# Kernel tuning notes

Hardware: AMD Instinct MI355X
Metric: run time of the kernel (lower is better)

The kernel has to match this reference:

```python
import jax, jax.numpy as jnp
import numpy as np

D_MODEL = 1024

def setup_inputs() -> dict:
    key = jax.random.key(0)
    ks = jax.random.split(key, 5)
    s = 1.0 / np.sqrt(D_MODEL)  # torch Linear default init scale-ish
    x = jax.random.normal(ks[0], (4, 2048, D_MODEL), dtype=jnp.float32)
    Wq = jax.random.normal(ks[1], (D_MODEL, D_MODEL), dtype=jnp.float32) * s
    Wk = jax.random.normal(ks[2], (D_MODEL, D_MODEL), dtype=jnp.float32) * s
    Wv = jax.random.normal(ks[3], (D_MODEL, D_MODEL), dtype=jnp.float32) * s
    Wo = jax.random.normal(ks[4], (D_MODEL, D_MODEL), dtype=jnp.float32) * s
    z = jnp.zeros((D_MODEL,), dtype=jnp.float32)
    return {"x": x, "Wq": Wq, "bq": z, "Wk": Wk, "bk": z, "Wv": Wv, "bv": z, "Wo": Wo, "bo": z}

def reference(x, Wq, bq, Wk, bk, Wv, bv, Wo, bo):
    # x: (B, S, D). Single-head causal attention, dropout in eval mode (identity).
    B, S, D = x.shape
    Q = jnp.einsum('bsd,ed->bse', x, Wq) + bq
    K = jnp.einsum('bsd,ed->bse', x, Wk) + bk
    V = jnp.einsum('bsd,ed->bse', x, Wv) + bv
    scores = jnp.einsum('bqd,bkd->bqk', Q, K) / jnp.sqrt(jnp.float32(D))
    causal = jnp.tril(jnp.ones((S, S), dtype=bool))  # (S, S)
    scores = jnp.where(causal, scores, -jnp.inf)
    weights = jax.nn.softmax(scores, axis=-1)
    attended = jnp.einsum('bqk,bkd->bqd', weights, V)
    out = jnp.einsum('bsd,ed->bse', attended, Wo) + bo
    return out
```

## Files before the change

### kernel.cpp

```cpp
#include <hip/hip_runtime.h>
#include <cstdint>
#include <cstddef>


#define D_MODEL 1024
#define SEQ     2048
#define BATCH   4

typedef unsigned short u16;
typedef __bf16 bf16_t;
typedef bf16_t bf16x8 __attribute__((ext_vector_type(8)));
typedef float  f32x4  __attribute__((ext_vector_type(4)));
typedef u16    u16x4  __attribute__((ext_vector_type(4)));

__device__ __forceinline__ u16 f2bf(float x) {
  union { float f; uint32_t u; } v; v.f = x;
  uint32_t r = v.u + 0x7fffu + ((v.u >> 16) & 1u);
  return (u16)(r >> 16);
}

__device__ __forceinline__ void gload_lds16(const u16* g, u16* l) {
  __builtin_amdgcn_global_load_lds((__attribute__((address_space(1))) void*)g,
                                   (__attribute__((address_space(3))) void*)l,
                                   16, 0, 0);
}

template <bool ROWSUM>
__device__ __forceinline__ void gemm_core(const u16* __restrict__ Ablk,
                                          const u16* __restrict__ Bblk,
                                          int lda, int ldb, int ksteps32,
                                          u16* As, u16* Bs,
                                          f32x4 acc[4][4], f32x4* rs) {
  const int tid  = threadIdx.x;
  const int wave = tid >> 6, lane = tid & 63;
  const int wr = (wave >> 1) * 64, wc = (wave & 1) * 64;
  const int frow = lane & 15, kc = lane >> 4;
  const int ch0 = tid, ch1 = 256 + tid;
  const int m0 = ch0 >> 2, k80 = (((ch0 & 3) ^ ((m0 >> 1) & 3))) * 8;
  const int m1 = ch1 >> 2, k81 = (((ch1 & 3) ^ ((m1 >> 1) & 3))) * 8;
  int aoff[4], boff[4];
#pragma unroll
  for (int i = 0; i < 4; ++i) {
    const int ra = wr + i * 16 + frow;
    aoff[i] = (ra * 4 + (kc ^ ((ra >> 1) & 3))) * 8;
    const int rb = wc + i * 16 + frow;
    boff[i] = (rb * 4 + (kc ^ ((rb >> 1) & 3))) * 8;
  }
  bf16x8 ones;
  if (ROWSUM) {
#pragma unroll
    for (int r = 0; r < 8; ++r) ((u16*)&ones)[r] = 0x3F80;
  }

  for (int kt = 0; kt < ksteps32; ++kt) {
    __syncthreads();
    const int kb = kt * 32;
    gload_lds16(Ablk + m0 * lda + kb + k80, As + ch0 * 8);
    gload_lds16(Ablk + m1 * lda + kb + k81, As + ch1 * 8);
    gload_lds16(Bblk + m0 * ldb + kb + k80, Bs + ch0 * 8);
    gload_lds16(Bblk + m1 * ldb + kb + k81, Bs + ch1 * 8);
    asm volatile("s_waitcnt vmcnt(0)" ::: "memory");
    __syncthreads();

    bf16x8 af[4], bf[4];
#pragma unroll
    for (int i = 0; i < 4; ++i) af[i] = *(const bf16x8*)(As + aoff[i]);
#pragma unroll
    for (int j = 0; j < 4; ++j) bf[j] = *(const bf16x8*)(Bs + boff[j]);
#pragma unroll
    for (int i = 0; i < 4; ++i)
#pragma unroll
      for (int j = 0; j < 4; ++j)
        acc[i][j] = __builtin_amdgcn_mfma_f32_16x16x32_bf16(af[i], bf[j], acc[i][j], 0, 0, 0);
    if (ROWSUM) {
#pragma unroll
      for (int i = 0; i < 4; ++i)
        rs[i] = __builtin_amdgcn_mfma_f32_16x16x32_bf16(af[i], ones, rs[i], 0, 0, 0);
    }
  }
}

__global__ __launch_bounds__(256) void cvt_kernel(const float4* __restrict__ x,
                                                  const float4* __restrict__ wq,
                                                  const float4* __restrict__ wk,
                                                  const float4* __restrict__ wv,
                                                  const float4* __restrict__ wo,
                                                  u16* __restrict__ dst) {
  const int i = blockIdx.x * 256 + threadIdx.x;
  float4 v;
  if (i < 2097152) {
    v = x[i];
  } else {
    const int j = i - 2097152;
    const int w = j >> 18;
    const float4* s = (w == 0) ? wq : (w == 1) ? wk : (w == 2) ? wv : wo;
    v = s[j & 262143];
  }
  u16x4 o = {f2bf(v.x), f2bf(v.y), f2bf(v.z), f2bf(v.w)};
  *(u16x4*)(dst + (size_t)i * 4) = o;
}

__global__ void transposeW_kernel(const u16* __restrict__ src, u16* __restrict__ dst) {
  __shared__ u16 tile[32][33];
  const int r0 = blockIdx.x * 32, c0 = blockIdx.y * 32;
  const int tx = threadIdx.x, ty = threadIdx.y;
#pragma unroll
  for (int r = 0; r < 4; ++r)
    tile[ty + r * 8][tx] = src[(size_t)(r0 + ty + r * 8) * D_MODEL + c0 + tx];
  __syncthreads();
#pragma unroll
  for (int r = 0; r < 4; ++r)
    dst[(size_t)(c0 + ty + r * 8) * D_MODEL + r0 + tx] = tile[tx][ty + r * 8];
}

__global__ __launch_bounds__(256) void stageA_kernel(
    const u16* __restrict__ xb,
    const u16* __restrict__ WqB, const u16* __restrict__ WkB,
    const u16* __restrict__ WoB, const u16* __restrict__ WvT,
    const float* __restrict__ Wo32, const float* __restrict__ bv,
    const float* __restrict__ bq, const float* __restrict__ bk,
    u16* __restrict__ Qb, u16* __restrict__ Kb,
    u16* __restrict__ Wp, float* __restrict__ bp) {
  __shared__ __align__(16) u16 As[4096];
  __shared__ __align__(16) u16 Bs[4096];
  const int blk = blockIdx.x;
  const int lane = threadIdx.x & 63, wave = threadIdx.x >> 6;
  const int wr = (wave >> 1) * 64, wc = (wave & 1) * 64;
  const int cl = lane & 15, rl = (lane >> 4) * 4;

  if (blk < 64) {
    const int f0 = (blk >> 3) * 128, e0 = (blk & 7) * 128;
    f32x4 acc[4][4] = {};
    gemm_core<false>(WoB + (size_t)f0 * D_MODEL, WvT + (size_t)e0 * D_MODEL,
                     D_MODEL, D_MODEL, 32, As, Bs, acc, nullptr);
#pragma unroll
    for (int j = 0; j < 4; ++j) {
      const int col = e0 + wc + j * 16 + cl;
#pragma unroll
      for (int i = 0; i < 4; ++i)
#pragma unroll
        for (int r = 0; r < 4; ++r) {
          const int row = f0 + wr + i * 16 + rl + r;
          Wp[(size_t)row * D_MODEL + col] = f2bf(acc[i][j][r]);
        }
    }
  } else if (blk < 80) {
    const int f = (blk - 64) * 64 + (threadIdx.x >> 2);
    const int dq = threadIdx.x & 3;
    const float* row = Wo32 + (size_t)f * D_MODEL + dq * 256;
    const float* bvq = bv + dq * 256;
    float s = 0.f;
#pragma unroll 8
    for (int i = 0; i < 256; ++i) s += row[i] * bvq[i];
    s += __shfl_xor(s, 1);
    s += __shfl_xor(s, 2);
    if (dq == 0) bp[f] = s;
  } else {
    const int v = blk - 80;
    const int c = v & 7, s = v >> 3;
    const int row0 = (c * 8 + (s >> 4)) * 128;
    const int cz = s & 15;
    const int z = cz >> 3;
    const int col0 = (cz & 7) * 128;
    const u16*   W    = z ? WkB : WqB;
    const float* bias = z ? bk : bq;
    u16*         out  = z ? Kb : Qb;
    f32x4 acc[4][4] = {};
    gemm_core<false>(xb + (size_t)row0 * D_MODEL, W + (size_t)col0 * D_MODEL,
                     D_MODEL, D_MODEL, 32, As, Bs, acc, nullptr);
#pragma unroll
    for (int j = 0; j < 4; ++j) {
      const int col = col0 + wc + j * 16 + cl;
      const float bb = bias[col];
#pragma unroll
      for (int i = 0; i < 4; ++i)
#pragma unroll
        for (int r = 0; r < 4; ++r) {
          const int row = row0 + wr + i * 16 + rl + r;
          out[(size_t)row * D_MODEL + col] = f2bf(acc[i][j][r] + bb);
        }
    }
  }
}

__global__ __launch_bounds__(256) void stageB_kernel(
    const u16* __restrict__ xb, const u16* __restrict__ Wp,
    const float* __restrict__ bp,
    const u16* __restrict__ Qb, const u16* __restrict__ Kb,
    u16* __restrict__ Vt, u16* __restrict__ Eb) {
  __shared__ __align__(16) u16 As[4096];
  __shared__ __align__(16) u16 Bs[4096];
  const int blk = blockIdx.x;
  const int lane = threadIdx.x & 63, wave = threadIdx.x >> 6;
  const int wr = (wave >> 1) * 64, wc = (wave & 1) * 64;
  const int cl = lane & 15, rl = (lane >> 4) * 4;

  if (blk < 544) {
    const int c = blk & 7, s = blk >> 3;
    int b, qi, ji;
    if (s < 48) {
      static const int sq_tab[6] = {1, 2, 2, 3, 3, 3};
      static const int sj_tab[6] = {0, 0, 1, 0, 1, 2};
      const int fi = c * 3 + (s >> 4);
      const int off = s & 15;
      b = fi / 6;
      const int fs = fi % 6;
      qi = sq_tab[fs] * 4 + (off >> 2);
      ji = sj_tab[fs] * 4 + (off & 3);
    } else {
      static const int di_tab[10] = {0, 1, 1, 2, 2, 2, 3, 3, 3, 3};
      static const int dj_tab[10] = {0, 0, 1, 0, 1, 2, 0, 1, 2, 3};
      const int k = (s - 48) / 10;
      const int off = (s - 48) % 10;
      const int di = c * 2 + k;
      b = di >> 2;
      const int dk = di & 3;
      qi = dk * 4 + di_tab[off];
      ji = dk * 4 + dj_tab[off];
    }
    const u16* A  = Qb + (size_t)(b * SEQ + qi * 128) * D_MODEL;
    const u16* Bt = Kb + (size_t)(b * SEQ + ji * 128) * D_MODEL;
    f32x4 acc[4][4] = {};
    gemm_core<false>(A, Bt, D_MODEL, D_MODEL, 32, As, Bs, acc, nullptr);
    u16* out = Eb + (size_t)b * SEQ * SEQ;
#pragma unroll
    for (int i = 0; i < 4; ++i)
#pragma unroll
      for (int r = 0; r < 4; ++r) {
        const int q = qi * 128 + wr + i * 16 + rl + r;
#pragma unroll
        for (int j = 0; j < 4; ++j) {
          const int jj = ji * 128 + wc + j * 16 + cl;
          out[(size_t)q * SEQ + jj] =
              (jj <= q) ? f2bf(__expf(acc[i][j][r] * 0.03125f)) : (u16)0;
        }
      }
  } else {
    const int v = blk - 544;
    const int c = v & 7, s = v >> 3;
    const int row0 = (c * 8 + (s >> 3)) * 128;
    const int col0 = (s & 7) * 128;
    f32x4 acc[4][4] = {};
    gemm_core<false>(xb + (size_t)row0 * D_MODEL, Wp + (size_t)col0 * D_MODEL,
                     D_MODEL, D_MODEL, 32, As, Bs, acc, nullptr);
    const int b = row0 >> 11;
    u16* vt = Vt + (size_t)b * D_MODEL * SEQ;
#pragma unroll
    for (int j = 0; j < 4; ++j) {
      const int col = col0 + wc + j * 16 + cl;
      const float bb = bp[col];
#pragma unroll
      for (int i = 0; i < 4; ++i) {
        const int s0 = (row0 & 2047) + wr + i * 16 + rl;
        u16x4 o = {f2bf(acc[i][j][0] + bb), f2bf(acc[i][j][1] + bb),
                   f2bf(acc[i][j][2] + bb), f2bf(acc[i][j][3] + bb)};
        *(u16x4*)(vt + (size_t)col * SEQ + s0) = o;
      }
    }
  }
}

__global__ __launch_bounds__(256) void pv_kernel(const u16* __restrict__ Eb,
                                                 const u16* __restrict__ Vt,
                                                 const float* __restrict__ bo,
                                                 float* __restrict__ Out) {
  __shared__ __align__(16) u16 As[4096];
  __shared__ __align__(16) u16 Bs[4096];
  const int u = blockIdx.x;
  const int c = u & 7, s = u >> 3;
  const int b  = c >> 1;
  const int dt = (c & 1) * 4 + (s >> 4);
  const int qt = 15 - (s & 15);
  const u16* A  = Eb + (size_t)b * SEQ * SEQ + (size_t)(qt * 128) * SEQ;
  const u16* Bt = Vt + (size_t)b * D_MODEL * SEQ + (size_t)(dt * 128) * SEQ;
  f32x4 acc[4][4] = {};
  f32x4 rs[4] = {};
  gemm_core<true>(A, Bt, SEQ, SEQ, (qt + 1) * 4, As, Bs, acc, rs);
  const int lane = threadIdx.x & 63, wave = threadIdx.x >> 6;
  const int wr = (wave >> 1) * 64, wc = (wave & 1) * 64;
  const int cl = lane & 15, rl = (lane >> 4) * 4;
#pragma unroll
  for (int i = 0; i < 4; ++i)
#pragma unroll
    for (int r = 0; r < 4; ++r) {
      const float invl = 1.0f / rs[i][r];
      const int row = b * SEQ + qt * 128 + wr + i * 16 + rl + r;
#pragma unroll
      for (int j = 0; j < 4; ++j) {
        const int col = dt * 128 + wc + j * 16 + cl;
        Out[(size_t)row * D_MODEL + col] = acc[i][j][r] * invl + bo[col];
      }
    }
}

extern "C" void kernel_launch(void* const* d_in, const int* in_sizes, int n_in,
                              void* d_out, int out_size, void* d_ws, size_t ws_size,
                              hipStream_t stream) {
  const float* x  = (const float*)d_in[0];
  const float* Wq = (const float*)d_in[1];
  const float* bq = (const float*)d_in[2];
  const float* Wk = (const float*)d_in[3];
  const float* bk = (const float*)d_in[4];
  const float* Wv = (const float*)d_in[5];
  const float* bv = (const float*)d_in[6];
  const float* Wo = (const float*)d_in[7];
  const float* bo = (const float*)d_in[8];
  float* out = (float*)d_out;
  char* ws = (char*)d_ws;

  u16*   xb  = (u16*)(ws);
  u16*   Wb  = (u16*)(ws + (16u << 20));
  u16*   Qb  = (u16*)(ws + (24u << 20));
  u16*   Kb  = (u16*)(ws + (40u << 20));
  u16*   Vt  = (u16*)(ws + (56u << 20));
  u16*   Eb  = (u16*)(ws + (72u << 20));
  u16*   WvT = (u16*)(ws + (104u << 20));
  u16*   Wp  = (u16*)(ws + (106u << 20));
  float* bp  = (float*)(ws + (108u << 20));

  cvt_kernel<<<12288, 256, 0, stream>>>((const float4*)x, (const float4*)Wq,
                                        (const float4*)Wk, (const float4*)Wv,
                                        (const float4*)Wo, xb);
  transposeW_kernel<<<dim3(32, 32), dim3(32, 8), 0, stream>>>(Wb + (2u << 20), WvT);
  stageA_kernel<<<1104, 256, 0, stream>>>(xb, Wb, Wb + (1u << 20), Wb + (3u << 20),
                                          WvT, Wo, bv, bq, bk, Qb, Kb, Wp, bp);
  stageB_kernel<<<1056, 256, 0, stream>>>(xb, Wp, bp, Qb, Kb, Vt, Eb);
  pv_kernel<<<512, 256, 0, stream>>>(Eb, Vt, bo, out);
}
```

Before: 267.9 us.

## Pipeline GEMM core with 4-stage LDS ring and enlarge tiles to 128x256

The shared GEMM core now prefetches K-slices two steps ahead into a four-deep LDS ring using vmcnt-based waits, and raises wave priority around the MFMA block. Block tiles grow from 128x128 with 4 waves to 128x256 with 8 waves, and all three stages are remapped to the new tiling: stage A fuses the QK projection with the Wv·Wo and bias work, stage B merges triangular score tiles, and PV is rebalanced. The aim is to hide global-load latency, which the old single-buffered loop exposed, and to raise operand reuse per block. In exchange it uses much more LDS per block, which may limit occupancy, and the block-to-work mapping becomes more complex.

```diff
diff --git a/kernel.cpp b/kernel.cpp
--- a/kernel.cpp
+++ b/kernel.cpp
@@ -26,24 +26,26 @@
 }
 
 template <bool ROWSUM>
-__device__ __forceinline__ void gemm_core(const u16* __restrict__ Ablk,
-                                          const u16* __restrict__ Bblk,
-                                          int lda, int ldb, int ksteps32,
+__device__ __forceinline__ void gemm_core(const u16* __restrict__ A,
+                                          const u16* __restrict__ B,
+                                          int lda, int ldb, int nt,
                                           u16* As, u16* Bs,
                                           f32x4 acc[4][4], f32x4* rs) {
   const int tid  = threadIdx.x;
-  const int wave = tid >> 6, lane = tid & 63;
-  const int wr = (wave >> 1) * 64, wc = (wave & 1) * 64;
+  const int lane = tid & 63, wave = tid >> 6;
   const int frow = lane & 15, kc = lane >> 4;
-  const int ch0 = tid, ch1 = 256 + tid;
-  const int m0 = ch0 >> 2, k80 = (((ch0 & 3) ^ ((m0 >> 1) & 3))) * 8;
-  const int m1 = ch1 >> 2, k81 = (((ch1 & 3) ^ ((m1 >> 1) & 3))) * 8;
+  const int abase = (wave >> 2) * 64, bbase = (wave & 3) * 64;
+  const int ar = tid >> 2;
+  const int ac = (tid & 3) ^ ((ar >> 1) & 3);
+  const u16* Asrc  = A + (size_t)ar * lda + ac * 8;
+  const u16* Bsrc0 = B + (size_t)ar * ldb + ac * 8;
+  const u16* Bsrc1 = B + (size_t)(ar + 128) * ldb + ac * 8;
   int aoff[4], boff[4];
 #pragma unroll
   for (int i = 0; i < 4; ++i) {
-    const int ra = wr + i * 16 + frow;
+    const int ra = abase + i * 16 + frow;
     aoff[i] = (ra * 4 + (kc ^ ((ra >> 1) & 3))) * 8;
-    const int rb = wc + i * 16 + frow;
+    const int rb = bbase + i * 16 + frow;
     boff[i] = (rb * 4 + (kc ^ ((rb >> 1) & 3))) * 8;
   }
   bf16x8 ones;
@@ -51,22 +53,30 @@
 #pragma unroll
     for (int r = 0; r < 8; ++r) ((u16*)&ones)[r] = 0x3F80;
   }
-
-  for (int kt = 0; kt < ksteps32; ++kt) {
-    __syncthreads();
-    const int kb = kt * 32;
-    gload_lds16(Ablk + m0 * lda + kb + k80, As + ch0 * 8);
-    gload_lds16(Ablk + m1 * lda + kb + k81, As + ch1 * 8);
-    gload_lds16(Bblk + m0 * ldb + kb + k80, Bs + ch0 * 8);
-    gload_lds16(Bblk + m1 * ldb + kb + k81, Bs + ch1 * 8);
-    asm volatile("s_waitcnt vmcnt(0)" ::: "memory");
-    __syncthreads();
-
+  auto stage = [&](int t) {
+    u16* ab = As + (t & 3) * 4096;
+    u16* bb = Bs + (t & 3) * 8192;
+    const int kb = t * 32;
+    gload_lds16(Asrc + kb, ab + tid * 8);
+    gload_lds16(Bsrc0 + kb, bb + tid * 8);
+    gload_lds16(Bsrc1 + kb, bb + 4096 + tid * 8);
+  };
+  stage(0);
+  stage(1);
+  for (int t = 0; t < nt; ++t) {
+    if (t + 1 < nt) asm volatile("s_waitcnt vmcnt(3)" ::: "memory");
+    else            asm volatile("s_waitcnt vmcnt(0)" ::: "memory");
+    if (t + 2 < nt) stage(t + 2);
+    __builtin_amdgcn_s_barrier();
+    asm volatile("" ::: "memory");
+    const u16* ab = As + (t & 3) * 4096;
+    const u16* bb = Bs + (t & 3) * 8192;
     bf16x8 af[4], bf[4];
 #pragma unroll
-    for (int i = 0; i < 4; ++i) af[i] = *(const bf16x8*)(As + aoff[i]);
-#pragma unroll
-    for (int j = 0; j < 4; ++j) bf[j] = *(const bf16x8*)(Bs + boff[j]);
+    for (int i = 0; i < 4; ++i) af[i] = *(const bf16x8*)(ab + aoff[i]);
+#pragma unroll
+    for (int j = 0; j < 4; ++j) bf[j] = *(const bf16x8*)(bb + boff[j]);
+    __builtin_amdgcn_s_setprio(1);
 #pragma unroll
     for (int i = 0; i < 4; ++i)
 #pragma unroll
@@ -77,6 +87,8 @@
       for (int i = 0; i < 4; ++i)
         rs[i] = __builtin_amdgcn_mfma_f32_16x16x32_bf16(af[i], ones, rs[i], 0, 0, 0);
     }
+    __builtin_amdgcn_s_setprio(0);
+    __builtin_amdgcn_s_barrier();
   }
 }
 
@@ -113,7 +125,7 @@
     dst[(size_t)(c0 + ty + r * 8) * D_MODEL + r0 + tx] = tile[tx][ty + r * 8];
 }
 
-__global__ __launch_bounds__(256) void stageA_kernel(
+__global__ __launch_bounds__(512, 2) void stageA_kernel(
     const u16* __restrict__ xb,
     const u16* __restrict__ WqB, const u16* __restrict__ WkB,
     const u16* __restrict__ WoB, const u16* __restrict__ WvT,
@@ -121,47 +133,18 @@
     const float* __restrict__ bq, const float* __restrict__ bk,
     u16* __restrict__ Qb, u16* __restrict__ Kb,
     u16* __restrict__ Wp, float* __restrict__ bp) {
-  __shared__ __align__(16) u16 As[4096];
-  __shared__ __align__(16) u16 Bs[4096];
-  const int blk = blockIdx.x;
-  const int lane = threadIdx.x & 63, wave = threadIdx.x >> 6;
-  const int wr = (wave >> 1) * 64, wc = (wave & 1) * 64;
+  __shared__ __align__(16) u16 As[16384];
+  __shared__ __align__(16) u16 Bs[32768];
+  const int blk = blockIdx.x, tid = threadIdx.x;
+  const int lane = tid & 63, wave = tid >> 6;
+  const int abase = (wave >> 2) * 64, bbase = (wave & 3) * 64;
   const int cl = lane & 15, rl = (lane >> 4) * 4;
-
-  if (blk < 64) {
-    const int f0 = (blk >> 3) * 128, e0 = (blk & 7) * 128;
-    f32x4 acc[4][4] = {};
-    gemm_core<false>(WoB + (size_t)f0 * D_MODEL, WvT + (size_t)e0 * D_MODEL,
-                     D_MODEL, D_MODEL, 32, As, Bs, acc, nullptr);
-#pragma unroll
-    for (int j = 0; j < 4; ++j) {
-      const int col = e0 + wc + j * 16 + cl;
-#pragma unroll
-      for (int i = 0; i < 4; ++i)
-#pragma unroll
-        for (int r = 0; r < 4; ++r) {
-          const int row = f0 + wr + i * 16 + rl + r;
-          Wp[(size_t)row * D_MODEL + col] = f2bf(acc[i][j][r]);
-        }
-    }
-  } else if (blk < 80) {
-    const int f = (blk - 64) * 64 + (threadIdx.x >> 2);
-    const int dq = threadIdx.x & 3;
-    const float* row = Wo32 + (size_t)f * D_MODEL + dq * 256;
-    const float* bvq = bv + dq * 256;
-    float s = 0.f;
-#pragma unroll 8
-    for (int i = 0; i < 256; ++i) s += row[i] * bvq[i];
-    s += __shfl_xor(s, 1);
-    s += __shfl_xor(s, 2);
-    if (dq == 0) bp[f] = s;
-  } else {
-    const int v = blk - 80;
-    const int c = v & 7, s = v >> 3;
-    const int row0 = (c * 8 + (s >> 4)) * 128;
-    const int cz = s & 15;
-    const int z = cz >> 3;
-    const int col0 = (cz & 7) * 128;
+  const int c = blk & 7, i = blk >> 3;
+
+  {
+    const int rt   = c * 8 + (i & 7);
+    const int czi  = i >> 3;
+    const int row0 = rt * 128, col0 = (czi >> 1) * 256, z = czi & 1;
     const u16*   W    = z ? WkB : WqB;
     const float* bias = z ? bk : bq;
     u16*         out  = z ? Kb : Qb;
@@ -170,76 +153,95 @@
                      D_MODEL, D_MODEL, 32, As, Bs, acc, nullptr);
 #pragma unroll
     for (int j = 0; j < 4; ++j) {
-      const int col = col0 + wc + j * 16 + cl;
+      const int col = col0 + bbase + j * 16 + cl;
       const float bb = bias[col];
 #pragma unroll
-      for (int i = 0; i < 4; ++i)
+      for (int ii = 0; ii < 4; ++ii)
 #pragma unroll
         for (int r = 0; r < 4; ++r) {
-          const int row = row0 + wr + i * 16 + rl + r;
-          out[(size_t)row * D_MODEL + col] = f2bf(acc[i][j][r] + bb);
+          const int row = row0 + abase + ii * 16 + rl + r;
+          out[(size_t)row * D_MODEL + col] = f2bf(acc[ii][j][r] + bb);
         }
     }
   }
-}
-
-__global__ __launch_bounds__(256) void stageB_kernel(
+  if (i < 4) {
+    const int widx = c * 4 + i;
+    const int f0 = (widx >> 2) * 128, e0 = (widx & 3) * 256;
+    f32x4 acc[4][4] = {};
+    gemm_core<false>(WoB + (size_t)f0 * D_MODEL, WvT + (size_t)e0 * D_MODEL,
+                     D_MODEL, D_MODEL, 32, As, Bs, acc, nullptr);
+#pragma unroll
+    for (int j = 0; j < 4; ++j) {
+      const int col = e0 + bbase + j * 16 + cl;
+#pragma unroll
+      for (int ii = 0; ii < 4; ++ii)
+#pragma unroll
+        for (int r = 0; r < 4; ++r) {
+          const int row = f0 + abase + ii * 16 + rl + r;
+          Wp[(size_t)row * D_MODEL + col] = f2bf(acc[ii][j][r]);
+        }
+    }
+  } else if (i < 6) {
+    const int f  = (c * 2 + (i - 4)) * 64 + (tid >> 3);
+    const int dq = tid & 7;
+    const float* row = Wo32 + (size_t)f * D_MODEL + dq * 128;
+    const float* bvq = bv + dq * 128;
+    float s = 0.f;
+#pragma unroll 8
+    for (int k = 0; k < 128; ++k) s += row[k] * bvq[k];
+    s += __shfl_xor(s, 1);
+    s += __shfl_xor(s, 2);
+    s += __shfl_xor(s, 4);
+    if (dq == 0) bp[f] = s;
+  }
+}
+
+__global__ __launch_bounds__(512, 2) void stageB_kernel(
     const u16* __restrict__ xb, const u16* __restrict__ Wp,
     const float* __restrict__ bp,
     const u16* __restrict__ Qb, const u16* __restrict__ Kb,
     u16* __restrict__ Vt, u16* __restrict__ Eb) {
-  __shared__ __align__(16) u16 As[4096];
-  __shared__ __align__(16) u16 Bs[4096];
-  const int blk = blockIdx.x;
-  const int lane = threadIdx.x & 63, wave = threadIdx.x >> 6;
-  const int wr = (wave >> 1) * 64, wc = (wave & 1) * 64;
+  __shared__ __align__(16) u16 As[16384];
+  __shared__ __align__(16) u16 Bs[32768];
+  const int blk = blockIdx.x, tid = threadIdx.x;
+  const int lane = tid & 63, wave = tid >> 6;
+  const int abase = (wave >> 2) * 64, bbase = (wave & 3) * 64;
   const int cl = lane & 15, rl = (lane >> 4) * 4;
 
-  if (blk < 544) {
-    const int c = blk & 7, s = blk >> 3;
-    int b, qi, ji;
-    if (s < 48) {
-      static const int sq_tab[6] = {1, 2, 2, 3, 3, 3};
-      static const int sj_tab[6] = {0, 0, 1, 0, 1, 2};
-      const int fi = c * 3 + (s >> 4);
-      const int off = s & 15;
-      b = fi / 6;
-      const int fs = fi % 6;
-      qi = sq_tab[fs] * 4 + (off >> 2);
-      ji = sj_tab[fs] * 4 + (off & 3);
-    } else {
-      static const int di_tab[10] = {0, 1, 1, 2, 2, 2, 3, 3, 3, 3};
-      static const int dj_tab[10] = {0, 0, 1, 0, 1, 2, 0, 1, 2, 3};
-      const int k = (s - 48) / 10;
-      const int off = (s - 48) % 10;
-      const int di = c * 2 + k;
-      b = di >> 2;
-      const int dk = di & 3;
-      qi = dk * 4 + di_tab[off];
-      ji = dk * 4 + dj_tab[off];
-    }
-    const u16* A  = Qb + (size_t)(b * SEQ + qi * 128) * D_MODEL;
-    const u16* Bt = Kb + (size_t)(b * SEQ + ji * 128) * D_MODEL;
-    f32x4 acc[4][4] = {};
-    gemm_core<false>(A, Bt, D_MODEL, D_MODEL, 32, As, Bs, acc, nullptr);
-    u16* out = Eb + (size_t)b * SEQ * SEQ;
-#pragma unroll
-    for (int i = 0; i < 4; ++i)
-#pragma unroll
-      for (int r = 0; r < 4; ++r) {
-        const int q = qi * 128 + wr + i * 16 + rl + r;
-#pragma unroll
-        for (int j = 0; j < 4; ++j) {
-          const int jj = ji * 128 + wc + j * 16 + cl;
-          out[(size_t)q * SEQ + jj] =
-              (jj <= q) ? f2bf(__expf(acc[i][j][r] * 0.03125f)) : (u16)0;
+  if (blk < 256) {
+    const int c = blk & 7;
+    const int nunit = (blk < 224) ? 1 : 2;
+    int uid = (blk < 224) ? (blk >> 3) : (28 + ((blk - 224) >> 3) * 2);
+    for (int uu = 0; uu < nunit; ++uu, ++uid) {
+      const int w = c * 36 + uid;
+      const int b = w / 72;
+      int r = w % 72, qi = 0;
+#pragma unroll 1
+      for (; qi < 16; ++qi) { const int n = (qi >> 1) + 1; if (r < n) break; r -= n; }
+      const int ji = r;
+      const u16* A  = Qb + (size_t)(b * SEQ + qi * 128) * D_MODEL;
+      const u16* Bt = Kb + (size_t)(b * SEQ + ji * 256) * D_MODEL;
+      f32x4 acc[4][4] = {};
+      gemm_core<false>(A, Bt, D_MODEL, D_MODEL, 32, As, Bs, acc, nullptr);
+      u16* out = Eb + (size_t)b * SEQ * SEQ;
+#pragma unroll
+      for (int ii = 0; ii < 4; ++ii)
+#pragma unroll
+        for (int rr = 0; rr < 4; ++rr) {
+          const int q = qi * 128 + abase + ii * 16 + rl + rr;
+#pragma unroll
+          for (int j = 0; j < 4; ++j) {
+            const int jj = ji * 256 + bbase + j * 16 + cl;
+            out[(size_t)q * SEQ + jj] =
+                (jj <= q) ? f2bf(__expf(acc[ii][j][rr] * 0.03125f)) : (u16)0;
+          }
         }
-      }
+    }
   } else {
-    const int v = blk - 544;
+    const int v = blk - 256;
     const int c = v & 7, s = v >> 3;
-    const int row0 = (c * 8 + (s >> 3)) * 128;
-    const int col0 = (s & 7) * 128;
+    const int row0 = (c * 8 + (s >> 2)) * 128;
+    const int col0 = (s & 3) * 256;
     f32x4 acc[4][4] = {};
     gemm_core<false>(xb + (size_t)row0 * D_MODEL, Wp + (size_t)col0 * D_MODEL,
                      D_MODEL, D_MODEL, 32, As, Bs, acc, nullptr);
@@ -247,48 +249,48 @@
     u16* vt = Vt + (size_t)b * D_MODEL * SEQ;
 #pragma unroll
     for (int j = 0; j < 4; ++j) {
-      const int col = col0 + wc + j * 16 + cl;
+      const int col = col0 + bbase + j * 16 + cl;
       const float bb = bp[col];
 #pragma unroll
-      for (int i = 0; i < 4; ++i) {
-        const int s0 = (row0 & 2047) + wr + i * 16 + rl;
-        u16x4 o = {f2bf(acc[i][j][0] + bb), f2bf(acc[i][j][1] + bb),
-                   f2bf(acc[i][j][2] + bb), f2bf(acc[i][j][3] + bb)};
+      for (int ii = 0; ii < 4; ++ii) {
+        const int s0 = (row0 & 2047) + abase + ii * 16 + rl;
+        u16x4 o = {f2bf(acc[ii][j][0] + bb), f2bf(acc[ii][j][1] + bb),
+                   f2bf(acc[ii][j][2] + bb), f2bf(acc[ii][j][3] + bb)};
         *(u16x4*)(vt + (size_t)col * SEQ + s0) = o;
       }
     }
   }
 }
 
-__global__ __launch_bounds__(256) void pv_kernel(const u16* __restrict__ Eb,
-                                                 const u16* __restrict__ Vt,
-                                                 const float* __restrict__ bo,
-                                                 float* __restrict__ Out) {
-  __shared__ __align__(16) u16 As[4096];
-  __shared__ __align__(16) u16 Bs[4096];
-  const int u = blockIdx.x;
-  const int c = u & 7, s = u >> 3;
+__global__ __launch_bounds__(512, 2) void pv_kernel(const u16* __restrict__ Eb,
+                                                    const u16* __restrict__ Vt,
+                                                    const float* __restrict__ bo,
+                                                    float* __restrict__ Out) {
+  __shared__ __align__(16) u16 As[16384];
+  __shared__ __align__(16) u16 Bs[32768];
+  const int blk = blockIdx.x, tid = threadIdx.x;
+  const int c = blk & 7, i = blk >> 3;
   const int b  = c >> 1;
-  const int dt = (c & 1) * 4 + (s >> 4);
-  const int qt = 15 - (s & 15);
+  const int dt = (c & 1) * 2 + (i >> 4);
+  const int qt = i & 15;
   const u16* A  = Eb + (size_t)b * SEQ * SEQ + (size_t)(qt * 128) * SEQ;
-  const u16* Bt = Vt + (size_t)b * D_MODEL * SEQ + (size_t)(dt * 128) * SEQ;
+  const u16* Bt = Vt + (size_t)b * D_MODEL * SEQ + (size_t)(dt * 256) * SEQ;
   f32x4 acc[4][4] = {};
   f32x4 rs[4] = {};
   gemm_core<true>(A, Bt, SEQ, SEQ, (qt + 1) * 4, As, Bs, acc, rs);
-  const int lane = threadIdx.x & 63, wave = threadIdx.x >> 6;
-  const int wr = (wave >> 1) * 64, wc = (wave & 1) * 64;
+  const int lane = tid & 63, wave = tid >> 6;
+  const int abase = (wave >> 2) * 64, bbase = (wave & 3) * 64;
   const int cl = lane & 15, rl = (lane >> 4) * 4;
 #pragma unroll
-  for (int i = 0; i < 4; ++i)
+  for (int ii = 0; ii < 4; ++ii)
 #pragma unroll
     for (int r = 0; r < 4; ++r) {
-      const float invl = 1.0f / rs[i][r];
-      const int row = b * SEQ + qt * 128 + wr + i * 16 + rl + r;
+      const float invl = 1.0f / rs[ii][r];
+      const int row = b * SEQ + qt * 128 + abase + ii * 16 + rl + r;
 #pragma unroll
       for (int j = 0; j < 4; ++j) {
-        const int col = dt * 128 + wc + j * 16 + cl;
-        Out[(size_t)row * D_MODEL + col] = acc[i][j][r] * invl + bo[col];
+        const int col = dt * 256 + bbase + j * 16 + cl;
+        Out[(size_t)row * D_MODEL + col] = acc[ii][j][r] * invl + bo[col];
       }
     }
 }
@@ -322,8 +324,8 @@
                                         (const float4*)Wk, (const float4*)Wv,
                                         (const float4*)Wo, xb);
   transposeW_kernel<<<dim3(32, 32), dim3(32, 8), 0, stream>>>(Wb + (2u << 20), WvT);
-  stageA_kernel<<<1104, 256, 0, stream>>>(xb, Wb, Wb + (1u << 20), Wb + (3u << 20),
-                                          WvT, Wo, bv, bq, bk, Qb, Kb, Wp, bp);
-  stageB_kernel<<<1056, 256, 0, stream>>>(xb, Wp, bp, Qb, Kb, Vt, Eb);
-  pv_kernel<<<512, 256, 0, stream>>>(Eb, Vt, bo, out);
-}
+  stageA_kernel<<<512, 512, 0, stream>>>(xb, Wb, Wb + (1u << 20), Wb + (3u << 20),
+                                         WvT, Wo, bv, bq, bk, Qb, Kb, Wp, bp);
+  stageB_kernel<<<512, 512, 0, stream>>>(xb, Wp, bp, Qb, Kb, Vt, Eb);
+  pv_kernel<<<256, 512, 0, stream>>>(Eb, Vt, bo, out);
+}
```

Measured after the change: 324.0 us. 20.9% more time.

## Compute softmax row sums in score epilogue and rebalance PV tile order

Applied to the files above, without the earlier changes.

Softmax denominators are now accumulated in the QK^T epilogue: each exponentiated score is rounded to bf16, summed across lanes with shuffles, and added to a per-row buffer with atomics. This removes the extra ones-vector MFMAs the PV GEMM used to compute row sums. The PV grid is also reordered to pair short and long causal query tiles across the two halves of the launch, for better load balance. In exchange this adds a memset, float atomics with nondeterministic summation order, and a dependency on a workspace region at 20MB, which appears to overlap the Qb allocation starting at 24MB only if sized past 4MB (it is 32KB, so fine).

```diff
diff --git a/kernel.cpp b/kernel.cpp
--- a/kernel.cpp
+++ b/kernel.cpp
@@ -18,6 +18,10 @@
   uint32_t r = v.u + 0x7fffu + ((v.u >> 16) & 1u);
   return (u16)(r >> 16);
 }
+__device__ __forceinline__ float bf2f(u16 h) {
+  union { uint32_t u; float f; } v; v.u = (uint32_t)h << 16;
+  return v.f;
+}
 
 __device__ __forceinline__ void gload_lds16(const u16* g, u16* l) {
   __builtin_amdgcn_global_load_lds((__attribute__((address_space(1))) void*)g,
@@ -25,14 +29,14 @@
                                    16, 0, 0);
 }
 
-template <bool ROWSUM>
 __device__ __forceinline__ void gemm_core(const u16* __restrict__ Ablk,
                                           const u16* __restrict__ Bblk,
                                           int lda, int ldb, int ksteps32,
                                           u16* As, u16* Bs,
-                                          f32x4 acc[4][4], f32x4* rs) {
+                                          f32x4 acc[4][4]) {
   const int tid  = threadIdx.x;
-  const int wave = tid >> 6, lane = tid & 63;
+  const int lane = tid & 63;
+  const int wave = tid >> 6;
   const int wr = (wave >> 1) * 64, wc = (wave & 1) * 64;
   const int frow = lane & 15, kc = lane >> 4;
   const int ch0 = tid, ch1 = 256 + tid;
@@ -46,19 +50,13 @@
     const int rb = wc + i * 16 + frow;
     boff[i] = (rb * 4 + (kc ^ ((rb >> 1) & 3))) * 8;
   }
-  bf16x8 ones;
-  if (ROWSUM) {
-#pragma unroll
-    for (int r = 0; r < 8; ++r) ((u16*)&ones)[r] = 0x3F80;
-  }
-
   for (int kt = 0; kt < ksteps32; ++kt) {
     __syncthreads();
     const int kb = kt * 32;
-    gload_lds16(Ablk + m0 * lda + kb + k80, As + ch0 * 8);
-    gload_lds16(Ablk + m1 * lda + kb + k81, As + ch1 * 8);
-    gload_lds16(Bblk + m0 * ldb + kb + k80, Bs + ch0 * 8);
-    gload_lds16(Bblk + m1 * ldb + kb + k81, Bs + ch1 * 8);
+    gload_lds16(Ablk + (size_t)m0 * lda + kb + k80, As + ch0 * 8);
+    gload_lds16(Ablk + (size_t)m1 * lda + kb + k81, As + ch1 * 8);
+    gload_lds16(Bblk + (size_t)m0 * ldb + kb + k80, Bs + ch0 * 8);
+    gload_lds16(Bblk + (size_t)m1 * ldb + kb + k81, Bs + ch1 * 8);
     asm volatile("s_waitcnt vmcnt(0)" ::: "memory");
     __syncthreads();
 
@@ -72,11 +70,6 @@
 #pragma unroll
       for (int j = 0; j < 4; ++j)
         acc[i][j] = __builtin_amdgcn_mfma_f32_16x16x32_bf16(af[i], bf[j], acc[i][j], 0, 0, 0);
-    if (ROWSUM) {
-#pragma unroll
-      for (int i = 0; i < 4; ++i)
-        rs[i] = __builtin_amdgcn_mfma_f32_16x16x32_bf16(af[i], ones, rs[i], 0, 0, 0);
-    }
   }
 }
 
@@ -131,8 +124,8 @@
   if (blk < 64) {
     const int f0 = (blk >> 3) * 128, e0 = (blk & 7) * 128;
     f32x4 acc[4][4] = {};
-    gemm_core<false>(WoB + (size_t)f0 * D_MODEL, WvT + (size_t)e0 * D_MODEL,
-                     D_MODEL, D_MODEL, 32, As, Bs, acc, nullptr);
+    gemm_core(WoB + (size_t)f0 * D_MODEL, WvT + (size_t)e0 * D_MODEL,
+              D_MODEL, D_MODEL, 32, As, Bs, acc);
 #pragma unroll
     for (int j = 0; j < 4; ++j) {
       const int col = e0 + wc + j * 16 + cl;
@@ -166,8 +159,8 @@
     const float* bias = z ? bk : bq;
     u16*         out  = z ? Kb : Qb;
     f32x4 acc[4][4] = {};
-    gemm_core<false>(xb + (size_t)row0 * D_MODEL, W + (size_t)col0 * D_MODEL,
-                     D_MODEL, D_MODEL, 32, As, Bs, acc, nullptr);
+    gemm_core(xb + (size_t)row0 * D_MODEL, W + (size_t)col0 * D_MODEL,
+              D_MODEL, D_MODEL, 32, As, Bs, acc);
 #pragma unroll
     for (int j = 0; j < 4; ++j) {
       const int col = col0 + wc + j * 16 + cl;
@@ -187,7 +180,7 @@
     const u16* __restrict__ xb, const u16* __restrict__ Wp,
     const float* __restrict__ bp,
     const u16* __restrict__ Qb, const u16* __restrict__ Kb,
-    u16* __restrict__ Vt, u16* __restrict__ Eb) {
+    u16* __restrict__ Vt, u16* __restrict__ Eb, float* __restrict__ rssum) {
   __shared__ __align__(16) u16 As[4096];
   __shared__ __align__(16) u16 Bs[4096];
   const int blk = blockIdx.x;
@@ -221,19 +214,27 @@
     const u16* A  = Qb + (size_t)(b * SEQ + qi * 128) * D_MODEL;
     const u16* Bt = Kb + (size_t)(b * SEQ + ji * 128) * D_MODEL;
     f32x4 acc[4][4] = {};
-    gemm_core<false>(A, Bt, D_MODEL, D_MODEL, 32, As, Bs, acc, nullptr);
+    gemm_core(A, Bt, D_MODEL, D_MODEL, 32, As, Bs, acc);
     u16* out = Eb + (size_t)b * SEQ * SEQ;
+    float* rs = rssum + b * SEQ;
 #pragma unroll
     for (int i = 0; i < 4; ++i)
 #pragma unroll
       for (int r = 0; r < 4; ++r) {
         const int q = qi * 128 + wr + i * 16 + rl + r;
+        float ps = 0.f;
 #pragma unroll
         for (int j = 0; j < 4; ++j) {
           const int jj = ji * 128 + wc + j * 16 + cl;
-          out[(size_t)q * SEQ + jj] =
-              (jj <= q) ? f2bf(__expf(acc[i][j][r] * 0.03125f)) : (u16)0;
+          u16 h16 = (jj <= q) ? f2bf(__expf(acc[i][j][r] * 0.03125f)) : (u16)0;
+          out[(size_t)q * SEQ + jj] = h16;
+          ps += bf2f(h16);
         }
+        ps += __shfl_xor(ps, 1);
+        ps += __shfl_xor(ps, 2);
+        ps += __shfl_xor(ps, 4);
+        ps += __shfl_xor(ps, 8);
+        if (cl == 0) atomicAdd(&rs[q], ps);
       }
   } else {
     const int v = blk - 544;
@@ -241,8 +242,8 @@
     const int row0 = (c * 8 + (s >> 3)) * 128;
     const int col0 = (s & 7) * 128;
     f32x4 acc[4][4] = {};
-    gemm_core<false>(xb + (size_t)row0 * D_MODEL, Wp + (size_t)col0 * D_MODEL,
-                     D_MODEL, D_MODEL, 32, As, Bs, acc, nullptr);
+    gemm_core(xb + (size_t)row0 * D_MODEL, Wp + (size_t)col0 * D_MODEL,
+              D_MODEL, D_MODEL, 32, As, Bs, acc);
     const int b = row0 >> 11;
     u16* vt = Vt + (size_t)b * D_MODEL * SEQ;
 #pragma unroll
@@ -262,20 +263,22 @@
 
 __global__ __launch_bounds__(256) void pv_kernel(const u16* __restrict__ Eb,
                                                  const u16* __restrict__ Vt,
+                                                 const float* __restrict__ rssum,
                                                  const float* __restrict__ bo,
                                                  float* __restrict__ Out) {
   __shared__ __align__(16) u16 As[4096];
   __shared__ __align__(16) u16 Bs[4096];
-  const int u = blockIdx.x;
-  const int c = u & 7, s = u >> 3;
+  const int blk = blockIdx.x;
+  const int half = blk >> 8, idx = blk & 255;
+  const int c = idx & 7, s = idx >> 3;
   const int b  = c >> 1;
-  const int dt = (c & 1) * 4 + (s >> 4);
-  const int qt = 15 - (s & 15);
+  const int dt = (c & 1) * 4 + (s & 3);
+  const int m  = s >> 2;
+  const int qt = half ? (15 - 2 * m) : (2 * m);
   const u16* A  = Eb + (size_t)b * SEQ * SEQ + (size_t)(qt * 128) * SEQ;
   const u16* Bt = Vt + (size_t)b * D_MODEL * SEQ + (size_t)(dt * 128) * SEQ;
   f32x4 acc[4][4] = {};
-  f32x4 rs[4] = {};
-  gemm_core<true>(A, Bt, SEQ, SEQ, (qt + 1) * 4, As, Bs, acc, rs);
+  gemm_core(A, Bt, SEQ, SEQ, (qt + 1) * 4, As, Bs, acc);
   const int lane = threadIdx.x & 63, wave = threadIdx.x >> 6;
   const int wr = (wave >> 1) * 64, wc = (wave & 1) * 64;
   const int cl = lane & 15, rl = (lane >> 4) * 4;
@@ -283,12 +286,12 @@
   for (int i = 0; i < 4; ++i)
 #pragma unroll
     for (int r = 0; r < 4; ++r) {
-      const float invl = 1.0f / rs[i][r];
-      const int row = b * SEQ + qt * 128 + wr + i * 16 + rl + r;
+      const int row = qt * 128 + wr + i * 16 + rl + r;
+      const float invl = 1.0f / rssum[b * SEQ + row];
 #pragma unroll
       for (int j = 0; j < 4; ++j) {
         const int col = dt * 128 + wc + j * 16 + cl;
-        Out[(size_t)row * D_MODEL + col] = acc[i][j][r] * invl + bo[col];
+        Out[(size_t)(b * SEQ + row) * D_MODEL + col] = acc[i][j][r] * invl + bo[col];
       }
     }
 }
@@ -317,6 +320,7 @@
   u16*   WvT = (u16*)(ws + (104u << 20));
   u16*   Wp  = (u16*)(ws + (106u << 20));
   float* bp  = (float*)(ws + (108u << 20));
+  float* rssum = (float*)(ws + (20u << 20));
 
   cvt_kernel<<<12288, 256, 0, stream>>>((const float4*)x, (const float4*)Wq,
                                         (const float4*)Wk, (const float4*)Wv,
@@ -324,6 +328,7 @@
   transposeW_kernel<<<dim3(32, 32), dim3(32, 8), 0, stream>>>(Wb + (2u << 20), WvT);
   stageA_kernel<<<1104, 256, 0, stream>>>(xb, Wb, Wb + (1u << 20), Wb + (3u << 20),
                                           WvT, Wo, bv, bq, bk, Qb, Kb, Wp, bp);
-  stageB_kernel<<<1056, 256, 0, stream>>>(xb, Wp, bp, Qb, Kb, Vt, Eb);
-  pv_kernel<<<512, 256, 0, stream>>>(Eb, Vt, bo, out);
-}
+  hipMemsetAsync(rssum, 0, BATCH * SEQ * sizeof(float), stream);
+  stageB_kernel<<<1056, 256, 0, stream>>>(xb, Wp, bp, Qb, Kb, Vt, Eb, rssum);
+  pv_kernel<<<512, 256, 0, stream>>>(Eb, Vt, rssum, bo, out);
+}
```

After: 267.3 us. About the same (-0.2%).
